# Kernel tuning notes

Measured on AMD Instinct MI355X. Metric: run time of the kernel, lower is better.

Reference implementation:

```python
import jax, jax.numpy as jnp
import numpy as np

B, L, D, DF, E = 8, 2048, 256, 1024, 1


def _layer_norm(x, g, b):
    mu = jnp.mean(x, axis=-1, keepdims=True)
    var = jnp.mean((x - mu) ** 2, axis=-1, keepdims=True)
    return (x - mu) * jax.lax.rsqrt(var + 1e-5) * g + b


def _ema_scan(z, a):
    # diagonal linear SSM: h_t = a*h_{t-1} + (1-a)*z_t, scanned over seq axis
    def step(h, zt):
        h = a * h + (1.0 - a) * zt
        return h, h
    zT = jnp.swapaxes(z, 0, 1)  # [L,B,D]
    h0 = jnp.zeros((z.shape[0], z.shape[2]), z.dtype)
    _, hs = jax.lax.scan(step, h0, zT)
    return jnp.swapaxes(hs, 0, 1)


def _mamba_block(x, m, Win, a_logit, Wout):
    zg = (x * m) @ Win                      # [B,L,2D]
    z, g = jnp.split(zg, 2, axis=-1)
    h = _ema_scan(z, jax.nn.sigmoid(a_logit))
    return ((h * jax.nn.silu(g)) @ Wout) * m


def _graph_agg(x, m, A_list, We):
    out = jnp.zeros_like(x)
    for e in range(We.shape[0]):
        A = A_list[e]
        agg = jnp.einsum('bij,bjd->bid', A, x * m)  # neighbor aggregation
        deg = jnp.clip(jnp.sum(A, axis=-1, keepdims=True), 1.0, None)
        out = out + (agg / deg) @ We[e]
    return jax.nn.relu(out) * m


def _masked_gather(x, idx, vc):
    # emulate: x_out[b,:vc] = x[b, idx[b,:vc]]; x_out[b,vc:] = x[b,vc:]
    pos = jnp.arange(x.shape[1])[None, :]
    im = jnp.where(pos < vc, idx, pos)
    return jnp.take_along_axis(x, im[:, :, None], axis=1)


def _forward(node_embedding, adjacency, gm1_Win, gm1_a_logit, gm1_Wout, gm2_We,
             gm_Win, gm_a_logit, gm_Wout, gm_We, ln1_g, ln1_b, ln2_g, ln2_b,
             ffn_W1, ffn_b1, ffn_W2, ffn_b2, Wv, bv,
             node_mask, sorted_list, reverse_list):
    X = node_embedding
    m = node_mask[:, :, None].astype(X.dtype)
    vc = jnp.sum(node_mask, axis=1, keepdims=True)  # [B,1] valid counts
    A_list = [adjacency]
    outs = []
    for si, ri in zip(sorted_list, reverse_list):
        se = _masked_gather(X, si, vc)
        bo = _mamba_block(se, m, gm1_Win, gm1_a_logit, gm1_Wout)
        re = _masked_gather(bo, ri, vc)
        outs.append(_graph_agg(re, m, A_list, gm2_We))
    outs.append(_mamba_block(X, m, gm_Win, gm_a_logit, gm_Wout) +
                _graph_agg(X, m, A_list, gm_We))
    # stack(dim=-1) + permute(0,1,3,2) + reshape == concat along feature dim
    Y = jnp.concatenate(outs, axis=-1) @ Wv + bv
    X1 = X + _layer_norm(Y, ln1_g, ln1_b)        # AddNorm, pre_ln, eval (no dropout)
    Y2 = jax.nn.relu(X1 @ ffn_W1 + ffn_b1) @ ffn_W2 + ffn_b2
    return X1 + _layer_norm(Y2, ln2_g, ln2_b)


def setup_inputs() -> dict:
    key = jax.random.key(0)
    ks = jax.random.split(key, 20)
    X = jax.random.normal(ks[0], (B, L, D), jnp.float32)
    lengths = jax.random.randint(ks[1], (B,), L // 2, L + 1)
    pos = jnp.arange(L)[None, :]
    M = (pos < lengths[:, None]).astype(jnp.int32)
    A = (jax.random.uniform(ks[2], (B, L, L)) < 0.004).astype(jnp.float32)
    A = A * M[:, :, None].astype(jnp.float32) * M[:, None, :].astype(jnp.float32)
    inp = {'node_embedding': X, 'node_mask': M, 'adjacency': A}
    for i in range(3):
        u = jax.random.uniform(ks[3 + i], (B, L))
        u = jnp.where(pos < lengths[:, None], u, 2.0 + pos.astype(jnp.float32))
        si = jnp.argsort(u, axis=1).astype(jnp.int32)   # perm of [0,vc) in prefix
        ri = jnp.argsort(si, axis=1).astype(jnp.int32)  # inverse permutation
        inp['sorted_indices_%d' % i] = si
        inp['reverse_indices_%d' % i] = ri
    def w(k, shape):
        return 0.02 * jax.random.normal(k, shape, jnp.float32)
    inp.update(
        gm1_Win=w(ks[6], (D, 2 * D)), gm1_a_logit=w(ks[7], (D,)), gm1_Wout=w(ks[8], (D, D)),
        gm2_We=w(ks[9], (E, D, D)),
        gm_Win=w(ks[10], (D, 2 * D)), gm_a_logit=w(ks[11], (D,)), gm_Wout=w(ks[12], (D, D)),
        gm_We=w(ks[13], (E, D, D)),
        ln1_g=jnp.ones((D,), jnp.float32), ln1_b=jnp.zeros((D,), jnp.float32),
        ln2_g=jnp.ones((D,), jnp.float32), ln2_b=jnp.zeros((D,), jnp.float32),
        ffn_W1=w(ks[14], (D, DF)), ffn_b1=jnp.zeros((DF,), jnp.float32),
        ffn_W2=w(ks[15], (DF, D)), ffn_b2=jnp.zeros((D,), jnp.float32),
        Wv=w(ks[16], (4 * D, D)), bv=jnp.zeros((D,), jnp.float32),
    )
    return inp


def reference(node_embedding, node_mask, adjacency,
              sorted_indices_0, sorted_indices_1, sorted_indices_2,
              reverse_indices_0, reverse_indices_1, reverse_indices_2,
              gm1_Win, gm1_a_logit, gm1_Wout, gm2_We,
              gm_Win, gm_a_logit, gm_Wout, gm_We,
              ln1_g, ln1_b, ln2_g, ln2_b,
              ffn_W1, ffn_b1, ffn_W2, ffn_b2, Wv, bv):
    return _forward(node_embedding, adjacency, gm1_Win, gm1_a_logit, gm1_Wout, gm2_We,
                    gm_Win, gm_a_logit, gm_Wout, gm_We, ln1_g, ln1_b, ln2_g, ln2_b,
                    ffn_W1, ffn_b1, ffn_W2, ffn_b2, Wv, bv,
                    node_mask,
                    [sorted_indices_0, sorted_indices_1, sorted_indices_2],
                    [reverse_indices_0, reverse_indices_1, reverse_indices_2])
```

## Files before the change

### kernel.cpp

```cpp
#include <hip/hip_runtime.h>

typedef unsigned short u16;
typedef unsigned int u32;
typedef unsigned long long u64;

#define BB 8
#define LL 2048
#define DD 256
#define NB (BB * LL)
#define NBR 4
#define NRT (NBR * NB)
#define NCH 32
#define CHL (LL / NCH)
#define CAP 64

typedef __attribute__((ext_vector_type(8))) __bf16 bf16x8;
typedef __attribute__((ext_vector_type(4))) float f32x4;

__device__ __forceinline__ float b2f(u16 u) {
    union { u32 u; float f; } x; x.u = ((u32)u) << 16; return x.f;
}
__device__ __forceinline__ u16 f2b(float f) {
    union { float f; u32 u; } x; x.f = f;
    u32 r = (x.u >> 16) & 1u;
    x.u += 0x7FFFu + r;
    return (u16)(x.u >> 16);
}
__device__ __forceinline__ float sigm(float x) { return 1.f / (1.f + __expf(-x)); }

#define GLD(gp, lp) __builtin_amdgcn_global_load_lds( \
    (const __attribute__((address_space(1))) void*)(gp), \
    (__attribute__((address_space(3))) void*)(lp), 16, 0, 0)

struct TrArgs {
    const float* s[9];
    u16* d[9];
    int K[9], N[9], tr[9];
    int beg[11];
    const float* xsrc;
    const int* maskp;
    u16* xdst;
};
__global__ void transpose_all(TrArgs a) {
    int blk = blockIdx.x;
    int i = 0;
    while (blk >= a.beg[i + 1]) ++i;
    if (i == 9) {
        int g = (blk - a.beg[9]) * 256 + threadIdx.x;
        int r = g >> 6;
        float4 v = a.maskp[r] ? *(const float4*)(a.xsrc + (size_t)g * 4)
                              : (float4){0.f, 0.f, 0.f, 0.f};
        union { u64 q; u16 h[4]; } pk;
        pk.h[0] = f2b(v.x); pk.h[1] = f2b(v.y); pk.h[2] = f2b(v.z); pk.h[3] = f2b(v.w);
        *(u64*)(a.xdst + (size_t)g * 4) = pk.q;
        return;
    }
    int idx = (blk - a.beg[i]) * 256 + threadIdx.x;
    int K = a.K[i], N = a.N[i];
    if (idx >= K * N) return;
    if (a.tr[i]) {
        int k = idx / N, n = idx - k * N;
        a.d[i][(size_t)n * K + k] = f2b(a.s[i][idx]);
    } else {
        a.d[i][idx] = f2b(a.s[i][idx]);
    }
}

__global__ void csr_kernel(const float* __restrict__ Adj,
                           const int* __restrict__ ri0, const int* __restrict__ ri1,
                           const int* __restrict__ ri2,
                           int* __restrict__ csr4, int* __restrict__ cnt,
                           float* __restrict__ deg) {
    int w = threadIdx.x >> 6, lane = threadIdx.x & 63;
    int row = blockIdx.x * 4 + w;
    int rowb = row & ~(LL - 1);
    const float* arow = Adj + (size_t)row * LL;
    int base = 0;
    for (int c = 0; c < LL / 256; ++c) {
        float4 v = *(const float4*)(arow + c * 256 + lane * 4);
#pragma unroll
        for (int e = 0; e < 4; ++e) {
            float f = (e == 0) ? v.x : (e == 1) ? v.y : (e == 2) ? v.z : v.w;
            bool nz = (f != 0.f);
            u64 m = __ballot(nz);
            if (nz) {
                int pos = base + __popcll(m & ((1ull << lane) - 1ull));
                if (pos < CAP) {
                    int j = c * 256 + lane * 4 + e;
                    csr4[((size_t)(3 * NB + row)) * CAP + pos] = j;
                    csr4[((size_t)(0 * NB + row)) * CAP + pos] = ri0[rowb + j];
                    csr4[((size_t)(1 * NB + row)) * CAP + pos] = ri1[rowb + j];
                    csr4[((size_t)(2 * NB + row)) * CAP + pos] = ri2[rowb + j];
                }
            }
            base += __popcll(m);
        }
    }
    if (lane == 0) {
        cnt[row] = base < CAP ? base : CAP;
        deg[row] = (float)(base < 1 ? 1 : base);
    }
}

__global__ __launch_bounds__(256)
void gemm_win_kernel(const u16* __restrict__ Xb,
                     const int* __restrict__ si0, const int* __restrict__ si1,
                     const int* __restrict__ si2,
                     const u16* __restrict__ Bt1, const u16* __restrict__ Bt2,
                     u16* __restrict__ zbuf, u16* __restrict__ gbuf)
{
    __shared__ __align__(16) u16 As[2][128 * 32];
    __shared__ __align__(16) u16 Bs[2][128 * 32];
    int tid = threadIdx.x, lane = tid & 63;
    int w = tid >> 6, wm = w >> 1, wn = w & 1;
    int rowBase = blockIdx.x * 128, colBase = blockIdx.y * 128;
    const u16* Bt = (rowBase < 3 * NB) ? Bt1 : Bt2;

    const u16* pa[2];
    const u16* pb[2];
#pragma unroll
    for (int rep = 0; rep < 2; ++rep) {
        int s = rep * 256 + tid;
        int row = s >> 2, kk = (s & 3) << 3;
        int rg = rowBase + row;
        int br = rg >> 14, r = rg & (NB - 1), b = r >> 11, l = r & (LL - 1);
        int src = (br == 0) ? si0[r] : (br == 1) ? si1[r] : (br == 2) ? si2[r] : l;
        pa[rep] = Xb + ((size_t)(b << 11) + src) * DD + kk;
        pb[rep] = Bt + (size_t)(colBase + row) * 256 + kk;
    }

    f32x4 acc[4][4];
#pragma unroll
    for (int m = 0; m < 4; ++m)
#pragma unroll
        for (int n = 0; n < 4; ++n) acc[m][n] = (f32x4){0.f, 0.f, 0.f, 0.f};

#pragma unroll
    for (int rep = 0; rep < 2; ++rep) {
        int s = rep * 256 + tid;
        GLD(pa[rep], As[0] + s * 8);
        GLD(pb[rep], Bs[0] + s * 8);
    }
    int p = 0;
    for (int t = 0; t < 8; ++t) {
        if (t + 1 < 8) {
            int k0 = (t + 1) * 32;
#pragma unroll
            for (int rep = 0; rep < 2; ++rep) {
                int s = rep * 256 + tid;
                GLD(pa[rep] + k0, As[p ^ 1] + s * 8);
                GLD(pb[rep] + k0, Bs[p ^ 1] + s * 8);
            }
            asm volatile("s_waitcnt vmcnt(4)" ::: "memory");
        } else {
            asm volatile("s_waitcnt vmcnt(0)" ::: "memory");
        }
        __builtin_amdgcn_s_barrier();
        int kq = (lane >> 4) << 3;
        bf16x8 av[4], bw[4];
#pragma unroll
        for (int m = 0; m < 4; ++m)
            av[m] = *(const bf16x8*)(As[p] + (wm * 64 + m * 16 + (lane & 15)) * 32 + kq);
#pragma unroll
        for (int n = 0; n < 4; ++n)
            bw[n] = *(const bf16x8*)(Bs[p] + (wn * 64 + n * 16 + (lane & 15)) * 32 + kq);
#pragma unroll
        for (int m = 0; m < 4; ++m)
#pragma unroll
            for (int n = 0; n < 4; ++n)
                acc[m][n] = __builtin_amdgcn_mfma_f32_16x16x32_bf16(av[m], bw[n], acc[m][n], 0, 0, 0);
        __builtin_amdgcn_s_barrier();
        p ^= 1;
    }

    u16* Cz;
    int cb;
    if (colBase < 256) { Cz = zbuf; cb = colBase; }
    else               { Cz = gbuf; cb = colBase - 256; }
    int cBase = cb + wn * 64 + (lane & 15);
    int rBase = rowBase + wm * 64 + ((lane >> 4) << 2);
#pragma unroll
    for (int m = 0; m < 4; ++m)
#pragma unroll
        for (int n = 0; n < 4; ++n)
#pragma unroll
            for (int r = 0; r < 4; ++r)
                Cz[(size_t)(rBase + m * 16 + r) * 256 + (cBase + n * 16)] = f2b(acc[m][n][r]);
}

__global__ __launch_bounds__(256)
void gemm_kernel(const u16* __restrict__ A1, const u16* __restrict__ A2, int asplit,
                 const u16* __restrict__ Bt1, const u16* __restrict__ Bt2,
                 const u16* __restrict__ Bt3, int split1, int split2,
                 void* __restrict__ Cout, const float* __restrict__ bias,
                 int N, int K, int mode)
{
    __shared__ __align__(16) u16 As[2][128 * 32];
    __shared__ __align__(16) u16 Bs[2][128 * 32];
    int tid = threadIdx.x;
    int lane = tid & 63;
    int w = tid >> 6, wm = w >> 1, wn = w & 1;
    int rowBase = blockIdx.x * 128, colBase = blockIdx.y * 128;
    const u16* Bt = (rowBase < split1) ? Bt1 : (rowBase < split2) ? Bt2 : Bt3;
    const u16* Arow = (rowBase < asplit) ? A1 + (size_t)rowBase * K
                                         : A2 + (size_t)(rowBase - asplit) * K;

    const u16* pa[2];
    const u16* pb[2];
#pragma unroll
    for (int rep = 0; rep < 2; ++rep) {
        int s = rep * 256 + tid;
        int row = s >> 2, kk = (s & 3) << 3;
        pa[rep] = Arow + (size_t)row * K + kk;
        pb[rep] = Bt + (size_t)(colBase + row) * K + kk;
    }

    f32x4 acc[4][4];
#pragma unroll
    for (int m = 0; m < 4; ++m)
#pragma unroll
        for (int n = 0; n < 4; ++n) acc[m][n] = (f32x4){0.f, 0.f, 0.f, 0.f};

    int nt = K >> 5;
#pragma unroll
    for (int rep = 0; rep < 2; ++rep) {
        int s = rep * 256 + tid;
        GLD(pa[rep], As[0] + s * 8);
        GLD(pb[rep], Bs[0] + s * 8);
    }
    int p = 0;
    for (int t = 0; t < nt; ++t) {
        if (t + 1 < nt) {
            int k0 = (t + 1) << 5;
#pragma unroll
            for (int rep = 0; rep < 2; ++rep) {
                int s = rep * 256 + tid;
                GLD(pa[rep] + k0, As[p ^ 1] + s * 8);
                GLD(pb[rep] + k0, Bs[p ^ 1] + s * 8);
            }
            asm volatile("s_waitcnt vmcnt(4)" ::: "memory");
        } else {
            asm volatile("s_waitcnt vmcnt(0)" ::: "memory");
        }
        __builtin_amdgcn_s_barrier();
        int kq = (lane >> 4) << 3;
        bf16x8 av[4], bw[4];
#pragma unroll
        for (int m = 0; m < 4; ++m)
            av[m] = *(const bf16x8*)(As[p] + (wm * 64 + m * 16 + (lane & 15)) * 32 + kq);
#pragma unroll
        for (int n = 0; n < 4; ++n)
            bw[n] = *(const bf16x8*)(Bs[p] + (wn * 64 + n * 16 + (lane & 15)) * 32 + kq);
#pragma unroll
        for (int m = 0; m < 4; ++m)
#pragma unroll
            for (int n = 0; n < 4; ++n)
                acc[m][n] = __builtin_amdgcn_mfma_f32_16x16x32_bf16(av[m], bw[n], acc[m][n], 0, 0, 0);
        __builtin_amdgcn_s_barrier();
        p ^= 1;
    }

    int cBase = colBase + wn * 64 + (lane & 15);
    int rBase = rowBase + wm * 64 + ((lane >> 4) << 2);
    u16* C = (u16*)Cout;
    float bz[4];
#pragma unroll
    for (int n = 0; n < 4; ++n) bz[n] = bias ? bias[cBase + n * 16] : 0.f;
#pragma unroll
    for (int m = 0; m < 4; ++m)
#pragma unroll
        for (int n = 0; n < 4; ++n)
#pragma unroll
            for (int r = 0; r < 4; ++r) {
                float v = acc[m][n][r] + bz[n];
                if (mode == 1) v = v > 0.f ? v : 0.f;
                C[(size_t)(rBase + m * 16 + r) * N + (cBase + n * 16)] = f2b(v);
            }
}

__global__ __launch_bounds__(256)
void gemm_splitk2_kernel(const u16* __restrict__ A, const u16* __restrict__ Bt,
                         u16* __restrict__ C0, u16* __restrict__ C1)
{
    __shared__ __align__(16) u16 As[2][128 * 32];
    __shared__ __align__(16) u16 Bs[2][128 * 32];
    int tid = threadIdx.x;
    int lane = tid & 63;
    int w = tid >> 6, wm = w >> 1, wn = w & 1;
    int rowBase = blockIdx.x * 128, colBase = blockIdx.y * 128;
    int koff = blockIdx.z * 512;

    const u16* pa[2];
    const u16* pb[2];
#pragma unroll
    for (int rep = 0; rep < 2; ++rep) {
        int s = rep * 256 + tid;
        int row = s >> 2, kk = (s & 3) << 3;
        pa[rep] = A + (size_t)(rowBase + row) * 1024 + koff + kk;
        pb[rep] = Bt + (size_t)(colBase + row) * 1024 + koff + kk;
    }

    f32x4 acc[4][4];
#pragma unroll
    for (int m = 0; m < 4; ++m)
#pragma unroll
        for (int n = 0; n < 4; ++n) acc[m][n] = (f32x4){0.f, 0.f, 0.f, 0.f};

#pragma unroll
    for (int rep = 0; rep < 2; ++rep) {
        int s = rep * 256 + tid;
        GLD(pa[rep], As[0] + s * 8);
        GLD(pb[rep], Bs[0] + s * 8);
    }
    int p = 0;
    for (int t = 0; t < 16; ++t) {
        if (t + 1 < 16) {
            int k0 = (t + 1) << 5;
#pragma unroll
            for (int rep = 0; rep < 2; ++rep) {
                int s = rep * 256 + tid;
                GLD(pa[rep] + k0, As[p ^ 1] + s * 8);
                GLD(pb[rep] + k0, Bs[p ^ 1] + s * 8);
            }
            asm volatile("s_waitcnt vmcnt(4)" ::: "memory");
        } else {
            asm volatile("s_waitcnt vmcnt(0)" ::: "memory");
        }
        __builtin_amdgcn_s_barrier();
        int kq = (lane >> 4) << 3;
        bf16x8 av[4], bw[4];
#pragma unroll
        for (int m = 0; m < 4; ++m)
            av[m] = *(const bf16x8*)(As[p] + (wm * 64 + m * 16 + (lane & 15)) * 32 + kq);
#pragma unroll
        for (int n = 0; n < 4; ++n)
            bw[n] = *(const bf16x8*)(Bs[p] + (wn * 64 + n * 16 + (lane & 15)) * 32 + kq);
#pragma unroll
        for (int m = 0; m < 4; ++m)
#pragma unroll
            for (int n = 0; n < 4; ++n)
                acc[m][n] = __builtin_amdgcn_mfma_f32_16x16x32_bf16(av[m], bw[n], acc[m][n], 0, 0, 0);
        __builtin_amdgcn_s_barrier();
        p ^= 1;
    }

    u16* C = blockIdx.z ? C1 : C0;
    int cBase = colBase + wn * 64 + (lane & 15);
    int rBase = rowBase + wm * 64 + ((lane >> 4) << 2);
#pragma unroll
    for (int m = 0; m < 4; ++m)
#pragma unroll
        for (int n = 0; n < 4; ++n)
#pragma unroll
            for (int r = 0; r < 4; ++r)
                C[(size_t)(rBase + m * 16 + r) * 256 + (cBase + n * 16)] = f2b(acc[m][n][r]);
}

__global__ void scan_carry_kernel(const u16* __restrict__ z4, const float* __restrict__ alog1,
                                  const float* __restrict__ alog2, float* __restrict__ carry) {
    int bid = blockIdx.x;
    int br = bid >> 8, b = (bid >> 5) & 7, c = bid & 31;
    int d0 = threadIdx.x * 2;
    const float* al = (br < 3) ? alog1 : alog2;
    float aA = sigm(al[d0]), aB = sigm(al[d0 + 1]);
    float hA = 0.f, hB = 0.f;
    const u16* zp = z4 + ((size_t)(br * NB + b * LL + c * CHL) * DD) + d0;
    for (int t = 0; t < CHL; ++t) {
        u32 v = *(const u32*)(zp + (size_t)t * DD);
        hA = aA * hA + (1.f - aA) * b2f((u16)v);
        hB = aB * hB + (1.f - aB) * b2f((u16)(v >> 16));
    }
    carry[(size_t)bid * DD + d0] = hA;
    carry[(size_t)bid * DD + d0 + 1] = hB;
}

__global__ void scan_apply_kernel(const u16* __restrict__ z4, const u16* __restrict__ g4,
                                  const float* __restrict__ alog1, const float* __restrict__ alog2,
                                  const float* __restrict__ carry, u16* __restrict__ U4) {
    int bid = blockIdx.x;
    int br = bid >> 8, b = (bid >> 5) & 7, c = bid & 31;
    int d0 = threadIdx.x * 2;
    const float* al = (br < 3) ? alog1 : alog2;
    float aA = sigm(al[d0]), aB = sigm(al[d0 + 1]);
    float aPA = aA, aPB = aB;
#pragma unroll
    for (int i = 0; i < 6; ++i) { aPA *= aPA; aPB *= aPB; }
    float hA = 0.f, hB = 0.f;
    const float* cp = carry + ((size_t)((br * 8 + b) * 32)) * DD + d0;
    for (int cc = 0; cc < c; ++cc) {
        float2 cv = *(const float2*)(cp + (size_t)cc * DD);
        hA = cv.x + aPA * hA;
        hB = cv.y + aPB * hB;
    }
    size_t rowOff = ((size_t)(br * NB + b * LL + c * CHL)) * DD + d0;
    const u16* zp = z4 + rowOff;
    const u16* gp = g4 + rowOff;
    u16* up = U4 + rowOff;
    for (int t = 0; t < CHL; ++t) {
        u32 zv = *(const u32*)(zp + (size_t)t * DD);
        u32 gv = *(const u32*)(gp + (size_t)t * DD);
        float gA = b2f((u16)gv), gB = b2f((u16)(gv >> 16));
        hA = aA * hA + (1.f - aA) * b2f((u16)zv);
        hB = aB * hB + (1.f - aB) * b2f((u16)(zv >> 16));
        u32 o = (u32)f2b(hA * gA * sigm(gA)) | ((u32)f2b(hB * gB * sigm(gB)) << 16);
        *(u32*)(up + (size_t)t * DD) = o;
    }
}

__global__ void agg4_kernel(const u16* __restrict__ V5, const int* __restrict__ csr4,
                            const int* __restrict__ cnt, const float* __restrict__ deg,
                            const int* __restrict__ maskp, u16* __restrict__ Yin) {
    int tr = threadIdx.x & 31;
    int rsub = threadIdx.x >> 5;
    int rg = blockIdx.x * 8 + rsub;
    int br = rg >> 14, r = rg & (NB - 1), b = r >> 11;
    int n = cnt[r];
    const int* lst = csr4 + ((size_t)(br * NB + r)) * CAP;
    const u16* srcB = V5 + ((size_t)((br < 3 ? br : 4) * NB + (b << 11))) * DD + tr * 8;
    float acc[8] = {0.f, 0.f, 0.f, 0.f, 0.f, 0.f, 0.f, 0.f};
    int i = 0;
    for (; i + 4 <= n; i += 4) {
        int4 il = *(const int4*)(lst + i);
        union { uint4 q; u16 h[8]; } v0, v1, v2, v3;
        v0.q = *(const uint4*)(srcB + (size_t)il.x * DD);
        v1.q = *(const uint4*)(srcB + (size_t)il.y * DD);
        v2.q = *(const uint4*)(srcB + (size_t)il.z * DD);
        v3.q = *(const uint4*)(srcB + (size_t)il.w * DD);
#pragma unroll
        for (int k = 0; k < 8; ++k)
            acc[k] += b2f(v0.h[k]) + b2f(v1.h[k]) + b2f(v2.h[k]) + b2f(v3.h[k]);
    }
    for (; i < n; ++i) {
        int idx = lst[i];
        union { uint4 q; u16 h[8]; } v;
        v.q = *(const uint4*)(srcB + (size_t)idx * DD);
#pragma unroll
        for (int k = 0; k < 8; ++k) acc[k] += b2f(v.h[k]);
    }
    float inv = 1.f / deg[r];
    int msk = maskp[r];
    union { uint4 q; u16 h[8]; } mo;
    if (br == 3) mo.q = *(const uint4*)(V5 + ((size_t)(3 * NB + r)) * DD + tr * 8);
    union { uint4 q; u16 h[8]; } o;
#pragma unroll
    for (int k = 0; k < 8; ++k) {
        float v = acc[k] * inv;
        v = v > 0.f ? v : 0.f;
        if (br == 3) v += b2f(mo.h[k]);
        v = msk ? v : 0.f;
        o.h[k] = f2b(v);
    }
    *(uint4*)(Yin + (size_t)r * 1024 + (br << 8) + tr * 8) = o.q;
}

__global__ void ln1_kernel(const u16* __restrict__ Ya, const u16* __restrict__ Yb,
                           const float* __restrict__ bvp,
                           const float* __restrict__ X, const float* __restrict__ gp,
                           const float* __restrict__ bp, float* __restrict__ X1f,
                           u16* __restrict__ X1b) {
    int wv = threadIdx.x >> 6, lane = threadIdx.x & 63;
    int r = blockIdx.x * 4 + wv;
    int d0 = lane << 2;
    union { u64 q; u16 h[4]; } ya, yb;
    ya.q = *(const u64*)(Ya + (size_t)r * DD + d0);
    yb.q = *(const u64*)(Yb + (size_t)r * DD + d0);
    float4 bb = *(const float4*)(bvp + d0);
    float x[4];
#pragma unroll
    for (int k = 0; k < 4; ++k) x[k] = b2f(ya.h[k]) + b2f(yb.h[k]) + (&bb.x)[k];
    float s = x[0] + x[1] + x[2] + x[3];
#pragma unroll
    for (int o = 32; o > 0; o >>= 1) s += __shfl_xor(s, o, 64);
    float mu = s * (1.f / DD);
    float dx[4], ss = 0.f;
#pragma unroll
    for (int k = 0; k < 4; ++k) { dx[k] = x[k] - mu; ss += dx[k] * dx[k]; }
#pragma unroll
    for (int o = 32; o > 0; o >>= 1) ss += __shfl_xor(ss, o, 64);
    float rstd = rsqrtf(ss * (1.f / DD) + 1e-5f);
    float4 g4 = *(const float4*)(gp + d0);
    float4 b4 = *(const float4*)(bp + d0);
    float4 xv = *(const float4*)(X + (size_t)r * DD + d0);
    float o4[4];
    union { u64 q; u16 h[4]; } pk;
#pragma unroll
    for (int k = 0; k < 4; ++k) {
        float y = dx[k] * rstd * (&g4.x)[k] + (&b4.x)[k];
        o4[k] = (&xv.x)[k] + y;
        pk.h[k] = f2b(o4[k]);
    }
    *(float4*)(X1f + (size_t)r * DD + d0) = (float4){o4[0], o4[1], o4[2], o4[3]};
    *(u64*)(X1b + (size_t)r * DD + d0) = pk.q;
}

__global__ void ln2_kernel(const u16* __restrict__ Ya, const u16* __restrict__ Yb,
                           const float* __restrict__ b2p,
                           const float* __restrict__ X1f, const float* __restrict__ gp,
                           const float* __restrict__ bp, float* __restrict__ Out) {
    int wv = threadIdx.x >> 6, lane = threadIdx.x & 63;
    int r = blockIdx.x * 4 + wv;
    int d0 = lane << 2;
    union { u64 q; u16 h[4]; } ya, yb;
    ya.q = *(const u64*)(Ya + (size_t)r * DD + d0);
    yb.q = *(const u64*)(Yb + (size_t)r * DD + d0);
    float4 bb = *(const float4*)(b2p + d0);
    float x[4];
#pragma unroll
    for (int k = 0; k < 4; ++k) x[k] = b2f(ya.h[k]) + b2f(yb.h[k]) + (&bb.x)[k];
    float s = x[0] + x[1] + x[2] + x[3];
#pragma unroll
    for (int o = 32; o > 0; o >>= 1) s += __shfl_xor(s, o, 64);
    float mu = s * (1.f / DD);
    float dx[4], ss = 0.f;
#pragma unroll
    for (int k = 0; k < 4; ++k) { dx[k] = x[k] - mu; ss += dx[k] * dx[k]; }
#pragma unroll
    for (int o = 32; o > 0; o >>= 1) ss += __shfl_xor(ss, o, 64);
    float rstd = rsqrtf(ss * (1.f / DD) + 1e-5f);
    float4 g4 = *(const float4*)(gp + d0);
    float4 b4 = *(const float4*)(bp + d0);
    float4 xv = *(const float4*)(X1f + (size_t)r * DD + d0);
    float o4[4];
#pragma unroll
    for (int k = 0; k < 4; ++k)
        o4[k] = (&xv.x)[k] + dx[k] * rstd * (&g4.x)[k] + (&b4.x)[k];
    *(float4*)(Out + (size_t)r * DD + d0) = (float4){o4[0], o4[1], o4[2], o4[3]};
}

extern "C" void kernel_launch(void* const* d_in, const int* in_sizes, int n_in,
                              void* d_out, int out_size, void* d_ws, size_t ws_size,
                              hipStream_t stream) {
    const float* X      = (const float*)d_in[0];
    const int* maskp    = (const int*)d_in[1];
    const float* Adj    = (const float*)d_in[2];
    const int* si[3]    = { (const int*)d_in[3], (const int*)d_in[5], (const int*)d_in[7] };
    const int* ri[3]    = { (const int*)d_in[4], (const int*)d_in[6], (const int*)d_in[8] };
    const float* gm1_Win  = (const float*)d_in[9];
    const float* gm1_alog = (const float*)d_in[10];
    const float* gm1_Wout = (const float*)d_in[11];
    const float* gm2_We   = (const float*)d_in[12];
    const float* gm_Win   = (const float*)d_in[13];
    const float* gm_alog  = (const float*)d_in[14];
    const float* gm_Wout  = (const float*)d_in[15];
    const float* gm_We    = (const float*)d_in[16];
    const float* ln1_g    = (const float*)d_in[17];
    const float* ln1_b    = (const float*)d_in[18];
    const float* ln2_g    = (const float*)d_in[19];
    const float* ln2_b    = (const float*)d_in[20];
    const float* ffn_W1   = (const float*)d_in[21];
    const float* ffn_b1   = (const float*)d_in[22];
    const float* ffn_W2   = (const float*)d_in[23];
    const float* ffn_b2   = (const float*)d_in[24];
    const float* Wv       = (const float*)d_in[25];
    const float* bv       = (const float*)d_in[26];
    float* Out = (float*)d_out;

    char* ws = (char*)d_ws;
    size_t off = 0;
    auto alloc = [&](size_t bytes) { size_t o = off; off += (bytes + 255) & ~(size_t)255; return o; };

    u16* WinT1  = (u16*)(ws + alloc((size_t)512 * 256 * 2));
    u16* WinT   = (u16*)(ws + alloc((size_t)512 * 256 * 2));
    u16* WoutT  = (u16*)(ws + alloc((size_t)256 * 256 * 2));
    u16* WeT1   = (u16*)(ws + alloc((size_t)256 * 256 * 2));
    u16* WeT    = (u16*)(ws + alloc((size_t)256 * 256 * 2));
    u16* WvT    = (u16*)(ws + alloc((size_t)256 * 1024 * 2));
    u16* W1T    = (u16*)(ws + alloc((size_t)1024 * 256 * 2));
    u16* W2T    = (u16*)(ws + alloc((size_t)256 * 1024 * 2));
    u16* WoutL  = (u16*)(ws + alloc((size_t)256 * 256 * 2));
    u16* Wc1T   = (u16*)(ws + alloc((size_t)256 * 256 * 2));
    u16* Xb     = (u16*)(ws + alloc((size_t)NB * DD * 2));
    int* csr4 = (int*)(ws + alloc((size_t)4 * NB * CAP * 4));
    int* cnt = (int*)(ws + alloc((size_t)NB * 4));
    float* deg = (float*)(ws + alloc((size_t)NB * 4));
    float* carry = (float*)(ws + alloc((size_t)NBR * BB * NCH * DD * 4));
    u16* zbuf = (u16*)(ws + alloc((size_t)NRT * DD * 2));
    u16* gbuf = (u16*)(ws + alloc((size_t)NRT * DD * 2));
    u16* U4   = (u16*)(ws + alloc((size_t)4 * NB * DD * 2));
    u16* V5   = (u16*)(ws + alloc((size_t)5 * NB * DD * 2));
    u16* Yin  = (u16*)(ws + alloc((size_t)NB * 1024 * 2));
    u16* tmpYa  = (u16*)(ws + alloc((size_t)NB * DD * 2));
    u16* tmpYb  = (u16*)(ws + alloc((size_t)NB * DD * 2));
    float* X1f   = (float*)(ws + alloc((size_t)NB * DD * 4));
    u16* X1b     = (u16*)(ws + alloc((size_t)NB * DD * 2));
    u16* H       = (u16*)(ws + alloc((size_t)NB * 1024 * 2));
    u16* tmpY2a  = (u16*)(ws + alloc((size_t)NB * DD * 2));
    u16* tmpY2b  = (u16*)(ws + alloc((size_t)NB * DD * 2));
    (void)ws_size; (void)in_sizes; (void)n_in; (void)out_size;

    TrArgs ta;
    const float* srcs[9] = { gm1_Win, gm_Win, gm_Wout, gm2_We, gm_We, Wv, ffn_W1, ffn_W2, gm1_Wout };
    u16* dsts[9]         = { WinT1,   WinT,   WoutT,   WeT1,   WeT,   WvT, W1T,   W2T,    WoutL };
    int Ks[9] = { 256, 256, 256, 256, 256, 1024, 256, 1024, 256 };
    int Ns[9] = { 512, 512, 256, 256, 256, 256, 1024, 256, 256 };
    int trs[9] = { 1, 1, 1, 1, 1, 1, 1, 1, 0 };
    int cum = 0;
    for (int i = 0; i < 9; ++i) {
        ta.s[i] = srcs[i]; ta.d[i] = dsts[i]; ta.K[i] = Ks[i]; ta.N[i] = Ns[i]; ta.tr[i] = trs[i];
        ta.beg[i] = cum; cum += (Ks[i] * Ns[i]) / 256;
    }
    ta.beg[9] = cum; cum += NB * DD / 4 / 256;
    ta.beg[10] = cum;
    ta.xsrc = X; ta.maskp = maskp; ta.xdst = Xb;
    transpose_all<<<cum, 256, 0, stream>>>(ta);

    gemm_kernel<<<dim3(2, 2), 256, 0, stream>>>(
        WeT1, WeT1, 1 << 30, WoutL, WoutL, WoutL, 1 << 30, 1 << 30,
        (void*)Wc1T, nullptr, 256, 256, 2);

    csr_kernel<<<NB / 4, 256, 0, stream>>>(Adj, ri[0], ri[1], ri[2], csr4, cnt, deg);

    gemm_win_kernel<<<dim3(NRT / 128, 512 / 128), 256, 0, stream>>>(
        Xb, si[0], si[1], si[2], WinT1, WinT, zbuf, gbuf);

    scan_carry_kernel<<<NBR * BB * NCH, 128, 0, stream>>>(zbuf, gm1_alog, gm_alog, carry);
    scan_apply_kernel<<<NBR * BB * NCH, 128, 0, stream>>>(zbuf, gbuf, gm1_alog, gm_alog, carry, U4);

    gemm_kernel<<<dim3(5 * NB / 128, 2), 256, 0, stream>>>(
        U4, Xb, 4 * NB, Wc1T, WoutT, WeT, 3 * NB, 4 * NB,
        (void*)V5, nullptr, 256, 256, 2);

    agg4_kernel<<<NRT / 8, 256, 0, stream>>>(V5, csr4, cnt, deg, maskp, Yin);

    gemm_splitk2_kernel<<<dim3(NB / 128, 2, 2), 256, 0, stream>>>(Yin, WvT, tmpYa, tmpYb);

    ln1_kernel<<<NB / 4, 256, 0, stream>>>(tmpYa, tmpYb, bv, X, ln1_g, ln1_b, X1f, X1b);

    gemm_kernel<<<dim3(NB / 128, 8), 256, 0, stream>>>(
        X1b, X1b, 1 << 30, W1T, W1T, W1T, 1 << 30, 1 << 30,
        (void*)H, ffn_b1, 1024, 256, 1);

    gemm_splitk2_kernel<<<dim3(NB / 128, 2, 2), 256, 0, stream>>>(H, W2T, tmpY2a, tmpY2b);

    ln2_kernel<<<NB / 4, 256, 0, stream>>>(tmpY2a, tmpY2b, ffn_b2, X1f, ln2_g, ln2_b, Out);
}
```

Before: 257.5 us.

## Parallelize CSR build per row, double scan chunks, drop fp32 residual buffer

The CSR build now uses one 256-thread block per adjacency row: four waves each scan a 512-column segment and stage hits in LDS, then a prefix over the wave counts fixes each wave's output offset. The kernel is also launched before the small weight-combine GEMM. The EMA scan chunk count rises from 32 to 64, giving more blocks and shorter serial loops, but the carry-combine loop in the apply kernel gets longer. The fp32 residual X1f is removed, so ln2 reads the bf16 X1b, which cuts memory traffic but rounds the residual to bf16.

Result: no change. 253.3 us (-1.6%).

```diff
diff --git a/kernel.cpp b/kernel.cpp
--- a/kernel.cpp
+++ b/kernel.cpp
@@ -10,7 +10,7 @@
 #define NB (BB * LL)
 #define NBR 4
 #define NRT (NBR * NB)
-#define NCH 32
+#define NCH 64
 #define CHL (LL / NCH)
 #define CAP 64
 
@@ -71,13 +71,16 @@
                            const int* __restrict__ ri2,
                            int* __restrict__ csr4, int* __restrict__ cnt,
                            float* __restrict__ deg) {
+    __shared__ int lidx[4][CAP];
+    __shared__ int lcnt[4], pre[4], tot;
+    int row = blockIdx.x;
     int w = threadIdx.x >> 6, lane = threadIdx.x & 63;
-    int row = blockIdx.x * 4 + w;
     int rowb = row & ~(LL - 1);
-    const float* arow = Adj + (size_t)row * LL;
+    const float* aseg = Adj + (size_t)row * LL + w * 512;
     int base = 0;
-    for (int c = 0; c < LL / 256; ++c) {
-        float4 v = *(const float4*)(arow + c * 256 + lane * 4);
+#pragma unroll
+    for (int it = 0; it < 2; ++it) {
+        float4 v = *(const float4*)(aseg + it * 256 + lane * 4);
 #pragma unroll
         for (int e = 0; e < 4; ++e) {
             float f = (e == 0) ? v.x : (e == 1) ? v.y : (e == 2) ? v.z : v.w;
@@ -85,20 +88,36 @@
             u64 m = __ballot(nz);
             if (nz) {
                 int pos = base + __popcll(m & ((1ull << lane) - 1ull));
-                if (pos < CAP) {
-                    int j = c * 256 + lane * 4 + e;
-                    csr4[((size_t)(3 * NB + row)) * CAP + pos] = j;
-                    csr4[((size_t)(0 * NB + row)) * CAP + pos] = ri0[rowb + j];
-                    csr4[((size_t)(1 * NB + row)) * CAP + pos] = ri1[rowb + j];
-                    csr4[((size_t)(2 * NB + row)) * CAP + pos] = ri2[rowb + j];
-                }
+                if (pos < CAP) lidx[w][pos] = w * 512 + it * 256 + lane * 4 + e;
             }
             base += __popcll(m);
         }
     }
-    if (lane == 0) {
-        cnt[row] = base < CAP ? base : CAP;
-        deg[row] = (float)(base < 1 ? 1 : base);
+    if (lane == 0) lcnt[w] = base;
+    __syncthreads();
+    if (threadIdx.x == 0) {
+        int s = 0;
+#pragma unroll
+        for (int i = 0; i < 4; ++i) { pre[i] = s; s += lcnt[i]; }
+        tot = s;
+    }
+    __syncthreads();
+    int cw = lcnt[w]; if (cw > CAP) cw = CAP;
+    int pw = pre[w];
+    for (int i = lane; i < cw; i += 64) {
+        int gpos = pw + i;
+        if (gpos < CAP) {
+            int j = lidx[w][i];
+            csr4[((size_t)(3 * NB + row)) * CAP + gpos] = j;
+            csr4[((size_t)(0 * NB + row)) * CAP + gpos] = ri0[rowb + j];
+            csr4[((size_t)(1 * NB + row)) * CAP + gpos] = ri1[rowb + j];
+            csr4[((size_t)(2 * NB + row)) * CAP + gpos] = ri2[rowb + j];
+        }
+    }
+    if (threadIdx.x == 0) {
+        int t = tot;
+        cnt[row] = t < CAP ? t : CAP;
+        deg[row] = (float)(t < 1 ? 1 : t);
     }
 }
 
@@ -359,7 +378,7 @@
 __global__ void scan_carry_kernel(const u16* __restrict__ z4, const float* __restrict__ alog1,
                                   const float* __restrict__ alog2, float* __restrict__ carry) {
     int bid = blockIdx.x;
-    int br = bid >> 8, b = (bid >> 5) & 7, c = bid & 31;
+    int br = bid >> 9, b = (bid >> 6) & 7, c = bid & 63;
     int d0 = threadIdx.x * 2;
     const float* al = (br < 3) ? alog1 : alog2;
     float aA = sigm(al[d0]), aB = sigm(al[d0 + 1]);
@@ -378,15 +397,15 @@
                                   const float* __restrict__ alog1, const float* __restrict__ alog2,
                                   const float* __restrict__ carry, u16* __restrict__ U4) {
     int bid = blockIdx.x;
-    int br = bid >> 8, b = (bid >> 5) & 7, c = bid & 31;
+    int br = bid >> 9, b = (bid >> 6) & 7, c = bid & 63;
     int d0 = threadIdx.x * 2;
     const float* al = (br < 3) ? alog1 : alog2;
     float aA = sigm(al[d0]), aB = sigm(al[d0 + 1]);
     float aPA = aA, aPB = aB;
 #pragma unroll
-    for (int i = 0; i < 6; ++i) { aPA *= aPA; aPB *= aPB; }
+    for (int i = 0; i < 5; ++i) { aPA *= aPA; aPB *= aPB; }
     float hA = 0.f, hB = 0.f;
-    const float* cp = carry + ((size_t)((br * 8 + b) * 32)) * DD + d0;
+    const float* cp = carry + ((size_t)((br * 8 + b) * NCH)) * DD + d0;
     for (int cc = 0; cc < c; ++cc) {
         float2 cv = *(const float2*)(cp + (size_t)cc * DD);
         hA = cv.x + aPA * hA;
@@ -456,8 +475,7 @@
 __global__ void ln1_kernel(const u16* __restrict__ Ya, const u16* __restrict__ Yb,
                            const float* __restrict__ bvp,
                            const float* __restrict__ X, const float* __restrict__ gp,
-                           const float* __restrict__ bp, float* __restrict__ X1f,
-                           u16* __restrict__ X1b) {
+                           const float* __restrict__ bp, u16* __restrict__ X1b) {
     int wv = threadIdx.x >> 6, lane = threadIdx.x & 63;
     int r = blockIdx.x * 4 + wv;
     int d0 = lane << 2;
@@ -481,28 +499,26 @@
     float4 g4 = *(const float4*)(gp + d0);
     float4 b4 = *(const float4*)(bp + d0);
     float4 xv = *(const float4*)(X + (size_t)r * DD + d0);
-    float o4[4];
     union { u64 q; u16 h[4]; } pk;
 #pragma unroll
     for (int k = 0; k < 4; ++k) {
         float y = dx[k] * rstd * (&g4.x)[k] + (&b4.x)[k];
-        o4[k] = (&xv.x)[k] + y;
-        pk.h[k] = f2b(o4[k]);
-    }
-    *(float4*)(X1f + (size_t)r * DD + d0) = (float4){o4[0], o4[1], o4[2], o4[3]};
+        pk.h[k] = f2b((&xv.x)[k] + y);
+    }
     *(u64*)(X1b + (size_t)r * DD + d0) = pk.q;
 }
 
 __global__ void ln2_kernel(const u16* __restrict__ Ya, const u16* __restrict__ Yb,
                            const float* __restrict__ b2p,
-                           const float* __restrict__ X1f, const float* __restrict__ gp,
+                           const u16* __restrict__ X1b, const float* __restrict__ gp,
                            const float* __restrict__ bp, float* __restrict__ Out) {
     int wv = threadIdx.x >> 6, lane = threadIdx.x & 63;
     int r = blockIdx.x * 4 + wv;
     int d0 = lane << 2;
-    union { u64 q; u16 h[4]; } ya, yb;
+    union { u64 q; u16 h[4]; } ya, yb, x1;
     ya.q = *(const u64*)(Ya + (size_t)r * DD + d0);
     yb.q = *(const u64*)(Yb + (size_t)r * DD + d0);
+    x1.q = *(const u64*)(X1b + (size_t)r * DD + d0);
     float4 bb = *(const float4*)(b2p + d0);
     float x[4];
 #pragma unroll
@@ -519,11 +535,10 @@
     float rstd = rsqrtf(ss * (1.f / DD) + 1e-5f);
     float4 g4 = *(const float4*)(gp + d0);
     float4 b4 = *(const float4*)(bp + d0);
-    float4 xv = *(const float4*)(X1f + (size_t)r * DD + d0);
     float o4[4];
 #pragma unroll
     for (int k = 0; k < 4; ++k)
-        o4[k] = (&xv.x)[k] + dx[k] * rstd * (&g4.x)[k] + (&b4.x)[k];
+        o4[k] = b2f(x1.h[k]) + dx[k] * rstd * (&g4.x)[k] + (&b4.x)[k];
     *(float4*)(Out + (size_t)r * DD + d0) = (float4){o4[0], o4[1], o4[2], o4[3]};
 }
 
@@ -581,11 +596,10 @@
     u16* Yin  = (u16*)(ws + alloc((size_t)NB * 1024 * 2));
     u16* tmpYa  = (u16*)(ws + alloc((size_t)NB * DD * 2));
     u16* tmpYb  = (u16*)(ws + alloc((size_t)NB * DD * 2));
-    float* X1f   = (float*)(ws + alloc((size_t)NB * DD * 4));
-    u16* X1b     = (u16*)(ws + alloc((size_t)NB * DD * 2));
-    u16* H       = (u16*)(ws + alloc((size_t)NB * 1024 * 2));
-    u16* tmpY2a  = (u16*)(ws + alloc((size_t)NB * DD * 2));
-    u16* tmpY2b  = (u16*)(ws + alloc((size_t)NB * DD * 2));
+    u16* X1b    = (u16*)(ws + alloc((size_t)NB * DD * 2));
+    u16* H      = (u16*)(ws + alloc((size_t)NB * 1024 * 2));
+    u16* tmpY2a = (u16*)(ws + alloc((size_t)NB * DD * 2));
+    u16* tmpY2b = (u16*)(ws + alloc((size_t)NB * DD * 2));
     (void)ws_size; (void)in_sizes; (void)n_in; (void)out_size;
 
     TrArgs ta;
@@ -604,12 +618,12 @@
     ta.xsrc = X; ta.maskp = maskp; ta.xdst = Xb;
     transpose_all<<<cum, 256, 0, stream>>>(ta);
 
+    csr_kernel<<<NB, 256, 0, stream>>>(Adj, ri[0], ri[1], ri[2], csr4, cnt, deg);
+
     gemm_kernel<<<dim3(2, 2), 256, 0, stream>>>(
         WeT1, WeT1, 1 << 30, WoutL, WoutL, WoutL, 1 << 30, 1 << 30,
         (void*)Wc1T, nullptr, 256, 256, 2);
 
-    csr_kernel<<<NB / 4, 256, 0, stream>>>(Adj, ri[0], ri[1], ri[2], csr4, cnt, deg);
-
     gemm_win_kernel<<<dim3(NRT / 128, 512 / 128), 256, 0, stream>>>(
         Xb, si[0], si[1], si[2], WinT1, WinT, zbuf, gbuf);
 
@@ -624,7 +638,7 @@
 
     gemm_splitk2_kernel<<<dim3(NB / 128, 2, 2), 256, 0, stream>>>(Yin, WvT, tmpYa, tmpYb);
 
-    ln1_kernel<<<NB / 4, 256, 0, stream>>>(tmpYa, tmpYb, bv, X, ln1_g, ln1_b, X1f, X1b);
+    ln1_kernel<<<NB / 4, 256, 0, stream>>>(tmpYa, tmpYb, bv, X, ln1_g, ln1_b, X1b);
 
     gemm_kernel<<<dim3(NB / 128, 8), 256, 0, stream>>>(
         X1b, X1b, 1 << 30, W1T, W1T, W1T, 1 << 30, 1 << 30,
@@ -632,5 +646,5 @@
 
     gemm_splitk2_kernel<<<dim3(NB / 128, 2, 2), 256, 0, stream>>>(H, W2T, tmpY2a, tmpY2b);
 
-    ln2_kernel<<<NB / 4, 256, 0, stream>>>(tmpY2a, tmpY2b, ffn_b2, X1f, ln2_g, ln2_b, Out);
-}
+    ln2_kernel<<<NB / 4, 256, 0, stream>>>(tmpY2a, tmpY2b, ffn_b2, X1b, ln2_g, ln2_b, Out);
+}
```
